# Performance work log

Measured on AMD Instinct MI355X. Metric: run time of the kernel, lower is better.

## Reference

```python
import jax, jax.numpy as jnp
import numpy as np
from jax import lax

KS = 11          # kernel_size
SIGMA = 1.5
MAX_VAL = 1.0
C1 = (0.01 * MAX_VAL) ** 2
C2 = (0.03 * MAX_VAL) ** 2
EPS = 1e-12
PAD = KS // 2    # use_padding=True -> reflect pad


def _gaussian_kernel3d():
    ax = jnp.arange(KS, dtype=jnp.float32) - (KS - 1) / 2.0
    g = jnp.exp(-(ax[:, None, None] ** 2 + ax[None, :, None] ** 2 + ax[None, None, :] ** 2)
                / (2.0 * SIGMA ** 2))
    return g / g.sum()  # (KS, KS, KS)


def setup_inputs() -> dict:
    key = jax.random.key(0)
    k1, k2 = jax.random.split(key)
    shape = (2, 1, 160, 160, 160)
    source = jax.random.uniform(k1, shape, dtype=jnp.float32)
    reference_vol = jax.random.uniform(k2, shape, dtype=jnp.float32)
    return {"source": source, "reference": reference_vol}


def reference(source, reference):
    B, C, H, W, D = source.shape
    # reflect pad spatial dims (torch 'reflect' == numpy 'reflect')
    pad_cfg = ((0, 0), (0, 0), (PAD, PAD), (PAD, PAD), (PAD, PAD))
    src = jnp.pad(source, pad_cfg, mode="reflect")
    ref = jnp.pad(reference, pad_cfg, mode="reflect")

    # fuse the 5 depthwise convolutions into one grouped conv over stacked channels
    stacked = jnp.concatenate([src, ref, src * src, ref * ref, src * ref], axis=1)  # (B,5C,...)
    kern = _gaussian_kernel3d()[None, None]                      # (1,1,KS,KS,KS)
    kern = jnp.tile(kern, (5 * C, 1, 1, 1, 1))                   # (5C,1,KS,KS,KS)
    out = lax.conv_general_dilated(
        stacked, kern, window_strides=(1, 1, 1), padding="VALID",
        feature_group_count=5 * C,
        dimension_numbers=("NCDHW", "OIDHW", "NCDHW"))           # (B,5C,H,W,D)

    mu1 = out[:, 0 * C:1 * C]
    mu2 = out[:, 1 * C:2 * C]
    m11 = out[:, 2 * C:3 * C]
    m22 = out[:, 3 * C:4 * C]
    m12 = out[:, 4 * C:5 * C]

    mu1_sq = mu1 * mu1
    mu2_sq = mu2 * mu2
    mu1_mu2 = mu1 * mu2
    sigma1_sq = m11 - mu1_sq
    sigma2_sq = m22 - mu2_sq
    sigma12 = m12 - mu1_mu2

    numerator = (2.0 * mu1_mu2 + C1) * (2.0 * sigma12 + C2)
    denominator = (mu1_sq + mu2_sq + C1) * (sigma1_sq + sigma2_sq + C2)
    ssim = numerator / (denominator + EPS)
    return 1.0 - ssim.mean()
```

## Files before the change

### kernel.cpp

```cpp
#include <hip/hip_runtime.h>
#include <math.h>

#define HH 160
#define WW 160
#define DD 160
#define VOL (HH*WW*DD)
#define KS 11
#define PAD 5
#define NBATCH 2
#define NTOT (NBATCH*VOL)

#define WT 16
#define DT 16
#define HT 32
#define WPN (WT + 2*PAD)
#define NP  (WPN * DT)
#define LROW (2*DT + 2)
#define LPLANE (WPN * LROW)
#define LBUF (3 * LPLANE)

struct Wts { float w[KS]; };

__device__ __forceinline__ int mirror(int i, int n) {
    if (i < 0) i = -i;
    if (i >= n) i = 2*n - 2 - i;
    return i;
}

__global__ void init_out(float* out) {
    if (threadIdx.x == 0 && blockIdx.x == 0) out[0] = 1.0f;
}

__global__ __launch_bounds__(256) void fused(const float* __restrict__ src,
                                             const float* __restrict__ ref,
                                             float* __restrict__ out,
                                             Wts wts, float scale) {
    __shared__ float sd[2][LBUF];

    const int bx  = blockIdx.x;
    const int dt_ = bx % (DD/DT);
    const int wt_ = (bx / (DD/DT)) % (WW/WT);
    const int ht_ = (bx / ((DD/DT)*(WW/WT))) % (HH/HT);
    const int b   = bx / ((DD/DT)*(WW/WT)*(HH/HT));
    const int d0 = dt_*DT, w0 = wt_*WT, h0 = ht_*HT;

    const int tid = threadIdx.x;
    const float* __restrict__ sp = src + (size_t)b*VOL;
    const float* __restrict__ rp = ref + (size_t)b*VOL;

    int tap0[KS], tap1[KS];
    int ws0, ws1;
    {
        int wp = tid / DT, dl = tid % DT;
        int wm = mirror(w0 - PAD + wp, WW);
        int da = d0 + dl;
#pragma unroll
        for (int k = 0; k < KS; ++k)
            tap0[k] = wm*DD + mirror(da - PAD + k, DD);
        ws0 = wp*LROW + 2*dl;
    }
    const int pi1 = tid + 256;
    const bool act1 = (pi1 < NP);
    {
        int pi = act1 ? pi1 : tid;
        int wp = pi / DT, dl = pi % DT;
        int wm = mirror(w0 - PAD + wp, WW);
        int da = d0 + dl;
#pragma unroll
        for (int k = 0; k < KS; ++k)
            tap1[k] = wm*DD + mirror(da - PAD + k, DD);
        ws1 = wp*LROW + 2*dl;
    }

    const int wl  = tid / DT;
    const int dl2 = tid % DT;
    const int rb  = wl*LROW + 2*dl2;

    float acc[5][KS];
#pragma unroll
    for (int c = 0; c < 5; ++c)
#pragma unroll
        for (int s = 0; s < KS; ++s) acc[c][s] = 0.f;

    float ssum = 0.f;
    const int NSTEP = HT + 2*PAD;

    for (int tb = 0; tb < 44; tb += 11) {
#pragma unroll
        for (int ts = 0; ts < 11; ++ts) {
            const int t = tb + ts;
            if (t < NSTEP) {
                const int hm = mirror(h0 - PAD + t, HH);
                const float* __restrict__ sh = sp + (size_t)hm*(WW*DD);
                const float* __restrict__ rh = rp + (size_t)hm*(WW*DD);
                float* __restrict__ buf = sd[t & 1];

                {
                    float mu1=0.f, mu2=0.f, m11=0.f, m22=0.f, m12=0.f;
#pragma unroll
                    for (int k = 0; k < KS; ++k) {
                        float s = sh[tap0[k]];
                        float r = rh[tap0[k]];
                        float wt = wts.w[k];
                        float p = wt*s, q = wt*r;
                        mu1 += p; mu2 += q;
                        m11 = fmaf(p, s, m11);
                        m22 = fmaf(q, r, m22);
                        m12 = fmaf(p, r, m12);
                    }
                    buf[ws0]              = mu1; buf[ws0+1]            = mu2;
                    buf[LPLANE + ws0]     = m11; buf[LPLANE + ws0+1]   = m22;
                    buf[2*LPLANE + ws0]   = m12;
                }
                if (act1) {
                    float mu1=0.f, mu2=0.f, m11=0.f, m22=0.f, m12=0.f;
#pragma unroll
                    for (int k = 0; k < KS; ++k) {
                        float s = sh[tap1[k]];
                        float r = rh[tap1[k]];
                        float wt = wts.w[k];
                        float p = wt*s, q = wt*r;
                        mu1 += p; mu2 += q;
                        m11 = fmaf(p, s, m11);
                        m22 = fmaf(q, r, m22);
                        m12 = fmaf(p, r, m12);
                    }
                    buf[ws1]              = mu1; buf[ws1+1]            = mu2;
                    buf[LPLANE + ws1]     = m11; buf[LPLANE + ws1+1]   = m22;
                    buf[2*LPLANE + ws1]   = m12;
                }
                __syncthreads();

                float v0=0.f, v1=0.f, v2=0.f, v3=0.f, v4=0.f;
#pragma unroll
                for (int k = 0; k < KS; ++k) {
                    const int o = rb + k*LROW;
                    const float wt = wts.w[k];
                    v0 = fmaf(wt, buf[o],              v0);
                    v1 = fmaf(wt, buf[o+1],            v1);
                    v2 = fmaf(wt, buf[LPLANE + o],     v2);
                    v3 = fmaf(wt, buf[LPLANE + o+1],   v3);
                    v4 = fmaf(wt, buf[2*LPLANE + o],   v4);
                }
#pragma unroll
                for (int m = 0; m < 11; ++m) {
                    const int slot = (ts + m) % 11;
                    const float wt = wts.w[10 - m];
                    acc[0][slot] = fmaf(wt, v0, acc[0][slot]);
                    acc[1][slot] = fmaf(wt, v1, acc[1][slot]);
                    acc[2][slot] = fmaf(wt, v2, acc[2][slot]);
                    acc[3][slot] = fmaf(wt, v3, acc[3][slot]);
                    acc[4][slot] = fmaf(wt, v4, acc[4][slot]);
                }
                if (t >= 10) {
                    float mu1 = acc[0][ts], mu2 = acc[1][ts];
                    float m11 = acc[2][ts], m22 = acc[3][ts], m12 = acc[4][ts];
                    float mu1sq = mu1*mu1, mu2sq = mu2*mu2, mu12 = mu1*mu2;
                    float s1 = m11 - mu1sq, s2 = m22 - mu2sq, s12 = m12 - mu12;
                    const float C1 = 1e-4f, C2 = 9e-4f;
                    float num = (2.f*mu12 + C1) * (2.f*s12 + C2);
                    float den = (mu1sq + mu2sq + C1) * (s1 + s2 + C2);
                    ssum += num / (den + 1e-12f);
                }
#pragma unroll
                for (int c = 0; c < 5; ++c) acc[c][ts] = 0.f;
            }
        }
    }

#pragma unroll
    for (int off = 32; off > 0; off >>= 1)
        ssum += __shfl_down(ssum, off, 64);
    __shared__ float lsum[4];
    int lane = tid & 63, wid = tid >> 6;
    if (lane == 0) lsum[wid] = ssum;
    __syncthreads();
    if (tid == 0)
        atomicAdd(out, -(lsum[0]+lsum[1]+lsum[2]+lsum[3]) * scale);
}

extern "C" void kernel_launch(void* const* d_in, const int* in_sizes, int n_in,
                              void* d_out, int out_size, void* d_ws, size_t ws_size,
                              hipStream_t stream) {
    const float* src = (const float*)d_in[0];
    const float* ref = (const float*)d_in[1];
    float* out = (float*)d_out;

    Wts wts;
    {
        double g[KS], s = 0.0;
        for (int i = 0; i < KS; ++i) {
            double a = (double)i - (KS - 1) / 2.0;
            g[i] = exp(-(a * a) / (2.0 * 1.5 * 1.5));
            s += g[i];
        }
        for (int i = 0; i < KS; ++i) wts.w[i] = (float)(g[i] / s);
    }

    const float scale = 1.0f / (float)NTOT;

    init_out<<<1, 64, 0, stream>>>(out);
    const int g = NBATCH * (HH/HT) * (WW/WT) * (DD/DT);
    fused<<<g, 256, 0, stream>>>(src, ref, out, wts, scale);
}
```

Baseline: 223.1 us.

## Stage raw H-planes in LDS with prefetched vector loads and packed FP32 math

Each thread now loads a float4 of source and reference per H-plane, interleaves them into a shared raw buffer, and the D-direction pass reads taps from LDS instead of issuing 11 scattered global gathers per output. The load for the next plane is issued before the barrier so it overlaps the W and H passes. The arithmetic uses v_pk_fma/v_pk_mul to process channel pairs together. Edge tiles in D take a separate mirrored-index path, and the per-plane double buffering is replaced by two barriers per step.

```diff
diff --git a/kernel.cpp b/kernel.cpp
--- a/kernel.cpp
+++ b/kernel.cpp
@@ -14,10 +14,13 @@
 #define DT 16
 #define HT 32
 #define WPN (WT + 2*PAD)
-#define NP  (WPN * DT)
-#define LROW (2*DT + 2)
-#define LPLANE (WPN * LROW)
-#define LBUF (3 * LPLANE)
+#define NSTEP (HT + 2*PAD)
+#define RS 68
+#define P01S 36
+#define P4S 17
+
+typedef float v2f __attribute__((ext_vector_type(2)));
+typedef float v4f __attribute__((ext_vector_type(4)));
 
 struct Wts { float w[KS]; };
 
@@ -27,6 +30,17 @@
     return i;
 }
 
+__device__ __forceinline__ v2f pk_fma(v2f a, v2f b, v2f c) {
+    v2f d;
+    asm("v_pk_fma_f32 %0, %1, %2, %3" : "=v"(d) : "v"(a), "v"(b), "v"(c));
+    return d;
+}
+__device__ __forceinline__ v2f pk_mul(v2f a, v2f b) {
+    v2f d;
+    asm("v_pk_mul_f32 %0, %1, %2" : "=v"(d) : "v"(a), "v"(b));
+    return d;
+}
+
 __global__ void init_out(float* out) {
     if (threadIdx.x == 0 && blockIdx.x == 0) out[0] = 1.0f;
 }
@@ -35,7 +49,10 @@
                                              const float* __restrict__ ref,
                                              float* __restrict__ out,
                                              Wts wts, float scale) {
-    __shared__ float sd[2][LBUF];
+    __shared__ float raw[WPN * RS];
+    __shared__ float pl01[WPN * P01S];
+    __shared__ float pl23[WPN * P01S];
+    __shared__ float pl4 [WPN * P4S];
 
     const int bx  = blockIdx.x;
     const int dt_ = bx % (DD/DT);
@@ -44,126 +61,163 @@
     const int b   = bx / ((DD/DT)*(WW/WT)*(HH/HT));
     const int d0 = dt_*DT, w0 = wt_*WT, h0 = ht_*HT;
 
+    const int  dbase = (d0 == 0) ? 0 : ((d0 == DD-DT) ? DD-32 : d0-8);
+    const bool dedge = (d0 == 0) || (d0 == DD-DT);
+
     const int tid = threadIdx.x;
     const float* __restrict__ sp = src + (size_t)b*VOL;
     const float* __restrict__ rp = ref + (size_t)b*VOL;
 
-    int tap0[KS], tap1[KS];
-    int ws0, ws1;
+    const bool sact = (tid < WPN*8);
+    const int  swp = tid >> 3, sq = tid & 7;
+    const int  sgoff  = mirror(w0 - PAD + (sact ? swp : 0), WW)*DD + dbase + sq*4;
+    const int  srawof = swp*RS + sq*8;
+
+    const int  p_dl  = tid & 15;
+    const int  p_wp0 = tid >> 4;
+    const bool p_act1 = (tid < WPN*DT - 256);
+    const int  pw0_01 = p_wp0*P01S + 2*p_dl;
+    const int  pw0_4  = p_wp0*P4S  + p_dl;
+    const int  pw1_01 = (p_wp0+16)*P01S + 2*p_dl;
+    const int  pw1_4  = (p_wp0+16)*P4S  + p_dl;
+
+    const int wl = tid >> 4, dl2 = tid & 15;
+
+    v2f wpk[KS];
+#pragma unroll
+    for (int k = 0; k < KS; ++k) { wpk[k].x = wts.w[k]; wpk[k].y = wts.w[k]; }
+
+    v2f acc01[KS], acc23[KS];
+    float acc4[KS];
+#pragma unroll
+    for (int s = 0; s < KS; ++s) {
+        acc01[s] = (v2f)0.f; acc23[s] = (v2f)0.f; acc4[s] = 0.f;
+    }
+
+    float ssum = 0.f;
+
+    v4f ra = (v4f)0.f, rb_ = (v4f)0.f;
     {
-        int wp = tid / DT, dl = tid % DT;
-        int wm = mirror(w0 - PAD + wp, WW);
-        int da = d0 + dl;
-#pragma unroll
-        for (int k = 0; k < KS; ++k)
-            tap0[k] = wm*DD + mirror(da - PAD + k, DD);
-        ws0 = wp*LROW + 2*dl;
-    }
-    const int pi1 = tid + 256;
-    const bool act1 = (pi1 < NP);
-    {
-        int pi = act1 ? pi1 : tid;
-        int wp = pi / DT, dl = pi % DT;
-        int wm = mirror(w0 - PAD + wp, WW);
-        int da = d0 + dl;
-#pragma unroll
-        for (int k = 0; k < KS; ++k)
-            tap1[k] = wm*DD + mirror(da - PAD + k, DD);
-        ws1 = wp*LROW + 2*dl;
-    }
-
-    const int wl  = tid / DT;
-    const int dl2 = tid % DT;
-    const int rb  = wl*LROW + 2*dl2;
-
-    float acc[5][KS];
-#pragma unroll
-    for (int c = 0; c < 5; ++c)
-#pragma unroll
-        for (int s = 0; s < KS; ++s) acc[c][s] = 0.f;
-
-    float ssum = 0.f;
-    const int NSTEP = HT + 2*PAD;
+        const int hm = mirror(h0 - PAD, HH);
+        if (sact) {
+            const float* g = sp + (size_t)hm*(WW*DD) + sgoff;
+            const float* h = rp + (size_t)hm*(WW*DD) + sgoff;
+            ra  = *reinterpret_cast<const v4f*>(g);
+            rb_ = *reinterpret_cast<const v4f*>(h);
+        }
+    }
 
     for (int tb = 0; tb < 44; tb += 11) {
 #pragma unroll
         for (int ts = 0; ts < 11; ++ts) {
             const int t = tb + ts;
             if (t < NSTEP) {
-                const int hm = mirror(h0 - PAD + t, HH);
-                const float* __restrict__ sh = sp + (size_t)hm*(WW*DD);
-                const float* __restrict__ rh = rp + (size_t)hm*(WW*DD);
-                float* __restrict__ buf = sd[t & 1];
+                if (sact) {
+                    v4f c0, c1;
+                    c0.x = ra.x; c0.y = rb_.x; c0.z = ra.y; c0.w = rb_.y;
+                    c1.x = ra.z; c1.y = rb_.z; c1.z = ra.w; c1.w = rb_.w;
+                    *reinterpret_cast<v4f*>(&raw[srawof])     = c0;
+                    *reinterpret_cast<v4f*>(&raw[srawof + 4]) = c1;
+                }
+                __syncthreads();
 
                 {
-                    float mu1=0.f, mu2=0.f, m11=0.f, m22=0.f, m12=0.f;
+                    v2f mu_a = (v2f)0.f, mm_a = (v2f)0.f;
+                    v2f mu_b = (v2f)0.f, mm_b = (v2f)0.f;
+                    float m12a = 0.f, m12b = 0.f;
+                    if (!dedge) {
+                        const float* r0 = &raw[p_wp0*RS + 2*(p_dl + 3)];
+                        const float* r1 = r0 + 16*RS;
+#pragma unroll
+                        for (int k = 0; k < KS; ++k) {
+                            v2f w  = wpk[k];
+                            v2f sr = *reinterpret_cast<const v2f*>(r0 + 2*k);
+                            mu_a = pk_fma(sr, w, mu_a);
+                            mm_a = pk_fma(pk_mul(sr, sr), w, mm_a);
+                            m12a = fmaf(w.x, sr.x*sr.y, m12a);
+                        }
+                        if (p_act1) {
+#pragma unroll
+                            for (int k = 0; k < KS; ++k) {
+                                v2f w  = wpk[k];
+                                v2f sr = *reinterpret_cast<const v2f*>(r1 + 2*k);
+                                mu_b = pk_fma(sr, w, mu_b);
+                                mm_b = pk_fma(pk_mul(sr, sr), w, mm_b);
+                                m12b = fmaf(w.x, sr.x*sr.y, m12b);
+                            }
+                        }
+                    } else {
+#pragma unroll
+                        for (int k = 0; k < KS; ++k) {
+                            const int widx = mirror(d0 + p_dl - PAD + k, DD) - dbase;
+                            v2f w  = wpk[k];
+                            v2f sr = *reinterpret_cast<const v2f*>(&raw[p_wp0*RS + 2*widx]);
+                            mu_a = pk_fma(sr, w, mu_a);
+                            mm_a = pk_fma(pk_mul(sr, sr), w, mm_a);
+                            m12a = fmaf(w.x, sr.x*sr.y, m12a);
+                            if (p_act1) {
+                                v2f sr2 = *reinterpret_cast<const v2f*>(&raw[(p_wp0+16)*RS + 2*widx]);
+                                mu_b = pk_fma(sr2, w, mu_b);
+                                mm_b = pk_fma(pk_mul(sr2, sr2), w, mm_b);
+                                m12b = fmaf(w.x, sr2.x*sr2.y, m12b);
+                            }
+                        }
+                    }
+                    *reinterpret_cast<v2f*>(&pl01[pw0_01]) = mu_a;
+                    *reinterpret_cast<v2f*>(&pl23[pw0_01]) = mm_a;
+                    pl4[pw0_4] = m12a;
+                    if (p_act1) {
+                        *reinterpret_cast<v2f*>(&pl01[pw1_01]) = mu_b;
+                        *reinterpret_cast<v2f*>(&pl23[pw1_01]) = mm_b;
+                        pl4[pw1_4] = m12b;
+                    }
+                }
+
+                {
+                    const int tn = t + 1;
+                    if (sact && tn < NSTEP) {
+                        const int hm = mirror(h0 - PAD + tn, HH);
+                        const float* g = sp + (size_t)hm*(WW*DD) + sgoff;
+                        const float* h = rp + (size_t)hm*(WW*DD) + sgoff;
+                        ra  = *reinterpret_cast<const v4f*>(g);
+                        rb_ = *reinterpret_cast<const v4f*>(h);
+                    }
+                }
+                __syncthreads();
+
+                {
+                    v2f v01 = (v2f)0.f, v23 = (v2f)0.f;
+                    float v4v = 0.f;
+                    const float* q01 = &pl01[wl*P01S + 2*dl2];
+                    const float* q23 = &pl23[wl*P01S + 2*dl2];
+                    const float* q4  = &pl4 [wl*P4S  + dl2];
 #pragma unroll
                     for (int k = 0; k < KS; ++k) {
-                        float s = sh[tap0[k]];
-                        float r = rh[tap0[k]];
-                        float wt = wts.w[k];
-                        float p = wt*s, q = wt*r;
-                        mu1 += p; mu2 += q;
-                        m11 = fmaf(p, s, m11);
-                        m22 = fmaf(q, r, m22);
-                        m12 = fmaf(p, r, m12);
-                    }
-                    buf[ws0]              = mu1; buf[ws0+1]            = mu2;
-                    buf[LPLANE + ws0]     = m11; buf[LPLANE + ws0+1]   = m22;
-                    buf[2*LPLANE + ws0]   = m12;
-                }
-                if (act1) {
-                    float mu1=0.f, mu2=0.f, m11=0.f, m22=0.f, m12=0.f;
-#pragma unroll
-                    for (int k = 0; k < KS; ++k) {
-                        float s = sh[tap1[k]];
-                        float r = rh[tap1[k]];
-                        float wt = wts.w[k];
-                        float p = wt*s, q = wt*r;
-                        mu1 += p; mu2 += q;
-                        m11 = fmaf(p, s, m11);
-                        m22 = fmaf(q, r, m22);
-                        m12 = fmaf(p, r, m12);
-                    }
-                    buf[ws1]              = mu1; buf[ws1+1]            = mu2;
-                    buf[LPLANE + ws1]     = m11; buf[LPLANE + ws1+1]   = m22;
-                    buf[2*LPLANE + ws1]   = m12;
-                }
-                __syncthreads();
-
-                float v0=0.f, v1=0.f, v2=0.f, v3=0.f, v4=0.f;
-#pragma unroll
-                for (int k = 0; k < KS; ++k) {
-                    const int o = rb + k*LROW;
-                    const float wt = wts.w[k];
-                    v0 = fmaf(wt, buf[o],              v0);
-                    v1 = fmaf(wt, buf[o+1],            v1);
-                    v2 = fmaf(wt, buf[LPLANE + o],     v2);
-                    v3 = fmaf(wt, buf[LPLANE + o+1],   v3);
-                    v4 = fmaf(wt, buf[2*LPLANE + o],   v4);
-                }
-#pragma unroll
-                for (int m = 0; m < 11; ++m) {
-                    const int slot = (ts + m) % 11;
-                    const float wt = wts.w[10 - m];
-                    acc[0][slot] = fmaf(wt, v0, acc[0][slot]);
-                    acc[1][slot] = fmaf(wt, v1, acc[1][slot]);
-                    acc[2][slot] = fmaf(wt, v2, acc[2][slot]);
-                    acc[3][slot] = fmaf(wt, v3, acc[3][slot]);
-                    acc[4][slot] = fmaf(wt, v4, acc[4][slot]);
-                }
-                if (t >= 10) {
-                    float mu1 = acc[0][ts], mu2 = acc[1][ts];
-                    float m11 = acc[2][ts], m22 = acc[3][ts], m12 = acc[4][ts];
-                    float mu1sq = mu1*mu1, mu2sq = mu2*mu2, mu12 = mu1*mu2;
-                    float s1 = m11 - mu1sq, s2 = m22 - mu2sq, s12 = m12 - mu12;
-                    const float C1 = 1e-4f, C2 = 9e-4f;
-                    float num = (2.f*mu12 + C1) * (2.f*s12 + C2);
-                    float den = (mu1sq + mu2sq + C1) * (s1 + s2 + C2);
-                    ssum += num / (den + 1e-12f);
-                }
-#pragma unroll
-                for (int c = 0; c < 5; ++c) acc[c][ts] = 0.f;
+                        v2f w = wpk[k];
+                        v01 = pk_fma(*reinterpret_cast<const v2f*>(q01 + k*P01S), w, v01);
+                        v23 = pk_fma(*reinterpret_cast<const v2f*>(q23 + k*P01S), w, v23);
+                        v4v = fmaf(w.x, q4[k*P4S], v4v);
+                    }
+#pragma unroll
+                    for (int m = 0; m < 11; ++m) {
+                        const int slot = (ts + m) % 11;
+                        v2f wt = wpk[10 - m];
+                        acc01[slot] = pk_fma(v01, wt, acc01[slot]);
+                        acc23[slot] = pk_fma(v23, wt, acc23[slot]);
+                        acc4[slot]  = fmaf(wt.x, v4v, acc4[slot]);
+                    }
+                    if (t >= 10) {
+                        float mu1 = acc01[ts].x, mu2 = acc01[ts].y;
+                        float m11 = acc23[ts].x, m22 = acc23[ts].y, m12 = acc4[ts];
+                        float mu1sq = mu1*mu1, mu2sq = mu2*mu2, mu12 = mu1*mu2;
+                        float s1 = m11 - mu1sq, s2 = m22 - mu2sq, s12 = m12 - mu12;
+                        const float C1 = 1e-4f, C2 = 9e-4f;
+                        float num = (2.f*mu12 + C1) * (2.f*s12 + C2);
+                        float den = (mu1sq + mu2sq + C1) * (s1 + s2 + C2);
+                        ssum += num / (den + 1e-12f);
+                    }
+                    acc01[ts] = (v2f)0.f; acc23[ts] = (v2f)0.f; acc4[ts] = 0.f;
+                }
             }
         }
     }
```

Result: faster. 213.0 us (-4.5%).
